# Optimization experiments

Measured on AMD Instinct MI355X. Metric: run time of the kernel, lower is better.

## Reference

```python
import jax, jax.numpy as jnp
import numpy as np

D = 1024
H = 8          # MHA fallback num_heads
DH = D // H
DFF = 4096     # mlp_ratio * hidden_size
EPS = 1e-6


def _ln(x, g, b):
    mu = jnp.mean(x, axis=-1, keepdims=True)
    var = jnp.mean((x - mu) ** 2, axis=-1, keepdims=True)
    return (x - mu) * jax.lax.rsqrt(var + EPS) * g + b


def setup_inputs() -> dict:
    key = jax.random.key(0)
    ks = jax.random.split(key, 16)
    s = 0.02
    return {
        "x": jax.random.normal(ks[0], (8, 1024, D), jnp.float32),
        "c": jax.random.normal(ks[1], (8, D), jnp.float32),
        # Mamba-block (attention fallback) params
        "m_ada_w": jax.random.normal(ks[2], (D, 3 * D), jnp.float32) * s,
        "m_ada_b": jnp.zeros((3 * D,), jnp.float32),
        "m_norm_g": jnp.ones((D,), jnp.float32),
        "m_norm_b": jnp.zeros((D,), jnp.float32),
        "in_proj_w": jax.random.normal(ks[3], (3 * D, D), jnp.float32) * s,
        "in_proj_b": jnp.zeros((3 * D,), jnp.float32),
        "out_proj_w": jax.random.normal(ks[4], (D, D), jnp.float32) * s,
        "out_proj_b": jnp.zeros((D,), jnp.float32),
        # FeedForward-block params
        "f_ada_w": jax.random.normal(ks[5], (D, 3 * D), jnp.float32) * s,
        "f_ada_b": jnp.zeros((3 * D,), jnp.float32),
        "f_norm_g": jnp.ones((D,), jnp.float32),
        "f_norm_b": jnp.zeros((D,), jnp.float32),
        "w1": jax.random.normal(ks[6], (D, DFF), jnp.float32) * s,
        "b1": jnp.zeros((DFF,), jnp.float32),
        "w2": jax.random.normal(ks[7], (DFF, D), jnp.float32) * s,
        "b2": jnp.zeros((D,), jnp.float32),
    }


def reference(x, c, m_ada_w, m_ada_b, m_norm_g, m_norm_b, in_proj_w, in_proj_b,
              out_proj_w, out_proj_b, f_ada_w, f_ada_b, f_norm_g, f_norm_b,
              w1, b1, w2, b2):
    B, N, _ = x.shape
    # ---- MambaBlock (MHA fallback), dropout = identity (eval) ----
    mod = jax.nn.silu(c) @ m_ada_w + m_ada_b              # (B, 3D)
    shift, scale, gate = jnp.split(mod, 3, axis=-1)
    h = _ln(x, m_norm_g, m_norm_b)
    h = h * (1.0 + scale[:, None, :]) + shift[:, None, :]
    qkv = h @ in_proj_w.T + in_proj_b                      # (B, N, 3D)
    q, k, v = jnp.split(qkv, 3, axis=-1)
    q = q.reshape(B, N, H, DH)
    k = k.reshape(B, N, H, DH)
    v = v.reshape(B, N, H, DH)
    scores = jnp.einsum("bqhd,bkhd->bhqk", q, k) / np.sqrt(DH).astype(np.float32)
    attn = jax.nn.softmax(scores, axis=-1)
    o = jnp.einsum("bhqk,bkhd->bqhd", attn, v).reshape(B, N, D)
    o = o @ out_proj_w.T + out_proj_b
    x = x + gate[:, None, :] * o
    # ---- FeedForward block ----
    mod2 = jax.nn.silu(c) @ f_ada_w + f_ada_b
    shift2, scale2, gate2 = jnp.split(mod2, 3, axis=-1)
    h = _ln(x, f_norm_g, f_norm_b)
    h = h * (1.0 + scale2[:, None, :]) + shift2[:, None, :]
    h = jax.nn.gelu(h @ w1 + b1, approximate=False) @ w2 + b2
    return x + gate2[:, None, :] * h
```

## Files before the change

### kernel.cpp

```cpp
#include <hip/hip_runtime.h>

typedef __bf16 bf16x8 __attribute__((ext_vector_type(8)));
typedef float f32x4 __attribute__((ext_vector_type(4)));

__device__ __forceinline__ unsigned short f2bf(float f) {
    unsigned int u = __float_as_uint(f);
    unsigned int r = (u + 0x7FFFu + ((u >> 16) & 1u)) >> 16;
    return (unsigned short)r;
}

__device__ __forceinline__ void gload16(const void* g, void* l) {
    __builtin_amdgcn_global_load_lds(
        (const __attribute__((address_space(1))) unsigned int*)g,
        (__attribute__((address_space(3))) unsigned int*)l, 16, 0, 0);
}

__device__ __forceinline__ void barrier_raw() {
    asm volatile("" ::: "memory");
    __builtin_amdgcn_s_barrier();
    asm volatile("" ::: "memory");
}

__device__ __forceinline__ void vmwait0() {
    asm volatile("s_waitcnt vmcnt(0)" ::: "memory");
}

__device__ __forceinline__ float gelu_fast(float u) {
    float z = 1.595769122f * u + 0.071354816f * u * u * u;
    return u / (1.f + __expf(-z));
}

__global__ __launch_bounds__(256) void f2b4(const float* __restrict__ in,
                                            unsigned short* __restrict__ out) {
    size_t i = ((size_t)blockIdx.x * 256 + threadIdx.x) * 4;
    float4 v = *(const float4*)(in + i);
    ushort4 o;
    o.x = f2bf(v.x); o.y = f2bf(v.y); o.z = f2bf(v.z); o.w = f2bf(v.w);
    *(ushort4*)(out + i) = o;
}

__global__ __launch_bounds__(256) void transpose_f2b(const float* __restrict__ in,
                                                     unsigned short* __restrict__ out,
                                                     int R, int C) {
    __shared__ float tile[32][33];
    int r0 = blockIdx.y * 32, c0 = blockIdx.x * 32;
    int tx = threadIdx.x & 31, ty = threadIdx.x >> 5;
#pragma unroll
    for (int i = 0; i < 4; i++) {
        int r = ty + i * 8;
        tile[r][tx] = in[(size_t)(r0 + r) * C + c0 + tx];
    }
    __syncthreads();
#pragma unroll
    for (int i = 0; i < 4; i++) {
        int r = ty + i * 8;
        out[(size_t)(c0 + r) * R + r0 + tx] = f2bf(tile[tx][r]);
    }
}

__global__ __launch_bounds__(256) void ada_mod_part(const float* __restrict__ c,
                                                    const float* __restrict__ W,
                                                    float* __restrict__ partial) {
    __shared__ float sc[8 * 64];
    int kc = blockIdx.y * 64;
    for (int i = threadIdx.x; i < 512; i += 256) {
        int b = i >> 6, k = i & 63;
        float cv = c[b * 1024 + kc + k];
        sc[i] = cv / (1.f + __expf(-cv));
    }
    __syncthreads();
    int j = blockIdx.x * 256 + threadIdx.x;
    float acc[8] = {0, 0, 0, 0, 0, 0, 0, 0};
    for (int k = 0; k < 64; k++) {
        float w = W[(size_t)(kc + k) * 3072 + j];
#pragma unroll
        for (int b = 0; b < 8; b++) acc[b] += sc[b * 64 + k] * w;
    }
#pragma unroll
    for (int b = 0; b < 8; b++) partial[((size_t)blockIdx.y * 8 + b) * 3072 + j] = acc[b];
}

__global__ __launch_bounds__(256) void ada_reduce(const float* __restrict__ partial,
                                                  const float* __restrict__ bias,
                                                  float* __restrict__ out) {
    int idx = blockIdx.x * 256 + threadIdx.x;
    int b = idx / 3072;
    int jj = idx - b * 3072;
    float s = bias[jj];
#pragma unroll
    for (int ch = 0; ch < 16; ch++) s += partial[((size_t)ch * 8 + b) * 3072 + jj];
    out[idx] = s;
}

__global__ __launch_bounds__(256) void ln_mod_kernel(const float* __restrict__ x,
                                                     const float* __restrict__ gamma,
                                                     const float* __restrict__ beta,
                                                     const float* __restrict__ mods,
                                                     unsigned short* __restrict__ out) {
    int row = blockIdx.x;
    int b = row >> 10;
    float4 v = ((const float4*)(x + (size_t)row * 1024))[threadIdx.x];
    float s = v.x + v.y + v.z + v.w;
    float s2 = v.x * v.x + v.y * v.y + v.z * v.z + v.w * v.w;
#pragma unroll
    for (int d = 1; d < 64; d <<= 1) { s += __shfl_xor(s, d); s2 += __shfl_xor(s2, d); }
    __shared__ float red[8];
    int lane = threadIdx.x & 63, wid = threadIdx.x >> 6;
    if (lane == 0) { red[wid] = s; red[4 + wid] = s2; }
    __syncthreads();
    float S = red[0] + red[1] + red[2] + red[3];
    float S2 = red[4] + red[5] + red[6] + red[7];
    float mu = S * (1.f / 1024.f);
    float var = S2 * (1.f / 1024.f) - mu * mu;
    float rs = rsqrtf(var + 1e-6f);
    const float* mrow = mods + b * 3072;
    int j0 = threadIdx.x * 4;
    float hv[4] = {v.x, v.y, v.z, v.w};
    ushort4 o;
    unsigned short* op = (unsigned short*)&o;
#pragma unroll
    for (int i = 0; i < 4; i++) {
        int j = j0 + i;
        float hh = (hv[i] - mu) * rs * gamma[j] + beta[j];
        hh = hh * (1.f + mrow[1024 + j]) + mrow[j];
        op[i] = f2bf(hh);
    }
    *(ushort4*)(out + (size_t)row * 1024 + j0) = o;
}

template <int NF, int EP>
__global__ __launch_bounds__(NF * 128, 4) void gemmo(const unsigned short* __restrict__ A,
                                                     const unsigned short* __restrict__ Bt,
                                                     int N, int K, int nx,
                                                     const float* __restrict__ bias,
                                                     const float* __restrict__ xres,
                                                     const float* __restrict__ mods,
                                                     float* __restrict__ outf,
                                                     unsigned short* __restrict__ outb,
                                                     unsigned short* __restrict__ vt) {
    constexpr int AE = 128 * 32;
    constexpr int BE = NF * 64 * 32;
    extern __shared__ __align__(16) char smem[];
    __bf16* As = (__bf16*)smem;
    __bf16* Bs = As + 2 * AE;

    int tid = threadIdx.x, lane = tid & 63, wid = tid >> 6;
    int wr, wc;
    if (NF == 4) { wr = wid >> 2; wc = wid & 3; }
    else         { wr = wid >> 1; wc = wid & 1; }
    int t = lane & 15, g = lane >> 4;
    int xk2 = ((t >> 1) & 3) * 8;

    int nwg = gridDim.x, chunk = nwg >> 3;
    int swz = (blockIdx.x & 7) * chunk + (blockIdx.x >> 3);
    int bx = swz % nx, by = swz / nx;
    int rowA0 = by * 128, colB0 = bx * (NF * 64);

    int rin = tid >> 2, cblk = tid & 3;
    int scol = (cblk ^ ((rin >> 1) & 3)) * 8;

    auto stage = [&](int nb, int kt) {
        int k0 = kt << 5;
        if (NF == 4) {
            gload16(A + (size_t)(rowA0 + rin) * K + k0 + scol, As + nb * AE + tid * 8);
            gload16(Bt + (size_t)(colB0 + rin) * K + k0 + scol, Bs + nb * BE + tid * 8);
            gload16(Bt + (size_t)(colB0 + 128 + rin) * K + k0 + scol,
                    Bs + nb * BE + 4096 + tid * 8);
        } else {
            gload16(A + (size_t)(rowA0 + rin) * K + k0 + scol, As + nb * AE + tid * 8);
            gload16(A + (size_t)(rowA0 + 64 + rin) * K + k0 + scol,
                    As + nb * AE + 2048 + tid * 8);
            gload16(Bt + (size_t)(colB0 + rin) * K + k0 + scol, Bs + nb * BE + tid * 8);
            gload16(Bt + (size_t)(colB0 + 64 + rin) * K + k0 + scol,
                    Bs + nb * BE + 2048 + tid * 8);
        }
    };

    f32x4 acc[4][4];
#pragma unroll
    for (int m = 0; m < 4; m++)
#pragma unroll
        for (int n = 0; n < 4; n++) acc[m][n] = (f32x4){0.f, 0.f, 0.f, 0.f};

    stage(0, 0);
    vmwait0();
    barrier_raw();

    int NT = K >> 5;
#pragma unroll 2
    for (int kt = 0; kt < NT; ++kt) {
        const __bf16* Ac = As + (kt & 1) * AE;
        const __bf16* Bc = Bs + (kt & 1) * BE;
        bool more = (kt + 1) < NT;
        if (more) stage((kt & 1) ^ 1, kt + 1);

        bf16x8 a[4], b[4];
#pragma unroll
        for (int m = 0; m < 4; m++)
            a[m] = *(const bf16x8*)&Ac[(wr * 64 + m * 16 + t) * 32 + ((g * 8) ^ xk2)];
#pragma unroll
        for (int n = 0; n < 4; n++)
            b[n] = *(const bf16x8*)&Bc[(wc * 64 + n * 16 + t) * 32 + ((g * 8) ^ xk2)];

        __builtin_amdgcn_s_setprio(1);
#pragma unroll
        for (int m = 0; m < 4; m++)
#pragma unroll
            for (int n = 0; n < 4; n++)
                acc[m][n] = __builtin_amdgcn_mfma_f32_16x16x32_bf16(a[m], b[n], acc[m][n], 0, 0, 0);
        __builtin_amdgcn_s_setprio(0);

        if (more) {
            vmwait0();
            barrier_raw();
        }
    }

    int row0 = rowA0 + wr * 64, col0 = colB0 + wc * 64;
    bool vpart = (EP == 0) && (colB0 >= 2048);
#pragma unroll
    for (int m = 0; m < 4; m++)
#pragma unroll
        for (int n = 0; n < 4; n++) {
            int col = col0 + n * 16 + t;
            if (EP == 0 && vpart) {
                int hcol = col - 2048;
                int hh = hcol >> 7, d = hcol & 127;
                int bb = row0 >> 10;
                int ntok = (row0 + m * 16 + g * 4) & 1023;
                float bs = bias[col];
                ushort4 vv;
                vv.x = f2bf(acc[m][n][0] + bs);
                vv.y = f2bf(acc[m][n][1] + bs);
                vv.z = f2bf(acc[m][n][2] + bs);
                vv.w = f2bf(acc[m][n][3] + bs);
                *(ushort4*)(vt + (((size_t)(bb * 8 + hh) * 128 + d) * 1024 + ntok)) = vv;
            } else {
#pragma unroll
                for (int r = 0; r < 4; r++) {
                    int row = row0 + m * 16 + g * 4 + r;
                    float v = acc[m][n][r];
                    if (EP == 0) {
                        outb[(size_t)row * N + col] = f2bf(v + bias[col]);
                    } else if (EP == 1) {
                        int bb = row >> 10;
                        float gt = mods[bb * 3072 + 2048 + col];
                        outf[(size_t)row * 1024 + col] =
                            xres[(size_t)row * 1024 + col] + gt * (v + bias[col]);
                    } else if (EP == 2) {
                        outb[(size_t)row * N + col] = f2bf(gelu_fast(v + bias[col]));
                    } else {
                        int bb = row >> 10;
                        float gt = mods[bb * 3072 + 2048 + col];
                        outf[(size_t)row * 1024 + col] += gt * (v + bias[col]);
                    }
                }
            }
        }
}

__global__ __launch_bounds__(512, 4) void attn_kernel(const unsigned short* __restrict__ qkv,
                                                      const unsigned short* __restrict__ vt,
                                                      unsigned short* __restrict__ o) {
    extern __shared__ __align__(16) char asmem[];
    __bf16* Ks = (__bf16*)asmem;
    __bf16* Vts = Ks + 2 * 64 * 128;

    int bid = blockIdx.x;
    int logical = (bid & 7) * 64 + (bid >> 3);
    int q0 = (logical & 7) * 128;
    int bh = logical >> 3;
    int b = bh >> 3, h = bh & 7;
    int tid = threadIdx.x, lane = tid & 63, w = tid >> 6;
    int t = lane & 15, g = lane >> 4;
    int swzt = (t & 7) << 4;

    const unsigned short* qbase = qkv + (size_t)(b * 1024) * 3072 + h * 128;
    int qrow = q0 + w * 16 + t;
    bf16x8 qf[4];
#pragma unroll
    for (int ks = 0; ks < 4; ks++)
        qf[ks] = *(const bf16x8*)(qbase + (size_t)qrow * 3072 + ks * 32 + g * 8);

    f32x4 Oa[8];
#pragma unroll
    for (int n = 0; n < 8; n++) Oa[n] = (f32x4){0.f, 0.f, 0.f, 0.f};
    float m_r = -1e30f, l_r = 0.f;
    const float scale = 0.08838834764831845f;

    int krow = tid >> 4;
    int ksrc = (((tid & 15) * 16) ^ ((krow & 7) << 4)) >> 1;
    int vrow = tid >> 3;
    int vsrc = (((tid & 7) * 16) ^ ((vrow & 7) << 4)) >> 1;
    const unsigned short* vtg = vt + (size_t)bh * 128 * 1024;

    auto stage = [&](int buf, int kv0) {
        const unsigned short* kb = qkv + (size_t)(b * 1024 + kv0) * 3072 + 1024 + h * 128;
#pragma unroll
        for (int cc = 0; cc < 2; cc++) {
            gload16(kb + (size_t)(cc * 32 + krow) * 3072 + ksrc,
                    (void*)(Ks + buf * 8192 + cc * 4096 + tid * 8));
            gload16(vtg + (size_t)(cc * 64 + vrow) * 1024 + kv0 + vsrc,
                    (void*)(Vts + buf * 8192 + cc * 4096 + tid * 8));
        }
    };

    stage(0, 0);
    vmwait0();
    barrier_raw();

#pragma unroll 1
    for (int tile = 0; tile < 16; ++tile) {
        int cur = tile & 1;
        bool more = tile < 15;
        if (more) stage(cur ^ 1, (tile + 1) * 64);
        const __bf16* Kc = Ks + cur * 8192;
        const __bf16* Vc = Vts + cur * 8192;

        f32x4 St[4];
#pragma unroll
        for (int n = 0; n < 4; n++) St[n] = (f32x4){0.f, 0.f, 0.f, 0.f};
        __builtin_amdgcn_s_setprio(1);
#pragma unroll
        for (int ks = 0; ks < 4; ks++) {
#pragma unroll
            for (int n = 0; n < 4; n++) {
                bf16x8 kf = *(const bf16x8*)&Kc[(n * 16 + t) * 128 + (((ks * 64 + g * 16) ^ swzt) >> 1)];
                St[n] = __builtin_amdgcn_mfma_f32_16x16x32_bf16(kf, qf[ks], St[n], 0, 0, 0);
            }
        }
        __builtin_amdgcn_s_setprio(0);

        float mx = -1e30f;
#pragma unroll
        for (int n = 0; n < 4; n++)
#pragma unroll
            for (int r = 0; r < 4; r++) mx = fmaxf(mx, St[n][r]);
        mx *= scale;
        mx = fmaxf(mx, __shfl_xor(mx, 16));
        mx = fmaxf(mx, __shfl_xor(mx, 32));
        float mn = fmaxf(m_r, mx);
        float alpha = __expf(m_r - mn);
        m_r = mn;
        float p[4][4];
        float rs = 0.f;
#pragma unroll
        for (int n = 0; n < 4; n++)
#pragma unroll
            for (int r = 0; r < 4; r++) {
                float pv = __expf(St[n][r] * scale - mn);
                p[n][r] = pv;
                rs += pv;
            }
        rs += __shfl_xor(rs, 16);
        rs += __shfl_xor(rs, 32);
        l_r = l_r * alpha + rs;

        unsigned P01[4], P23[4];
#pragma unroll
        for (int n = 0; n < 4; n++) {
            P01[n] = (unsigned)f2bf(p[n][0]) | ((unsigned)f2bf(p[n][1]) << 16);
            P23[n] = (unsigned)f2bf(p[n][2]) | ((unsigned)f2bf(p[n][3]) << 16);
        }

#pragma unroll
        for (int r = 0; r < 4; r++) {
            float ar = __shfl(alpha, (lane & 48) + g * 4 + r);
#pragma unroll
            for (int n2 = 0; n2 < 8; n2++) Oa[n2][r] *= ar;
        }

#pragma unroll
        for (int ks2 = 0; ks2 < 2; ks2++) {
            int e = ks2 * 2, od = ks2 * 2 + 1;
            unsigned s16a = (g < 2) ? P01[e] : P01[od];
            unsigned s16b = (g < 2) ? P23[e] : P23[od];
            unsigned s32a = (g & 1) ? P01[e] : P01[od];
            unsigned s32b = (g & 1) ? P23[e] : P23[od];
            unsigned s48a = (g >= 2) ? P01[e] : P01[od];
            unsigned s48b = (g >= 2) ? P23[e] : P23[od];
            unsigned r16a = __shfl_xor(s16a, 16), r16b = __shfl_xor(s16b, 16);
            unsigned r32a = __shfl_xor(s32a, 32), r32b = __shfl_xor(s32b, 32);
            unsigned r48a = __shfl_xor(s48a, 48), r48b = __shfl_xor(s48b, 48);
            union { unsigned u[4]; bf16x8 v; } pa;
            pa.u[0] = (g == 0) ? P01[e] : (g == 1) ? r48a : (g == 2) ? r32a : r16a;
            pa.u[1] = (g == 0) ? P23[e] : (g == 1) ? r48b : (g == 2) ? r32b : r16b;
            pa.u[2] = (g == 0) ? r16a : (g == 1) ? r32a : (g == 2) ? r48a : P01[od];
            pa.u[3] = (g == 0) ? r16b : (g == 1) ? r32b : (g == 2) ? r48b : P23[od];
            __builtin_amdgcn_s_setprio(1);
#pragma unroll
            for (int n2 = 0; n2 < 8; n2++) {
                bf16x8 vf = *(const bf16x8*)&Vc[(n2 * 16 + t) * 64 + (((ks2 * 64 + g * 16) ^ swzt) >> 1)];
                Oa[n2] = __builtin_amdgcn_mfma_f32_16x16x32_bf16(pa.v, vf, Oa[n2], 0, 0, 0);
            }
            __builtin_amdgcn_s_setprio(0);
        }

        if (more) {
            vmwait0();
            barrier_raw();
        }
    }

#pragma unroll
    for (int r = 0; r < 4; r++) {
        float lq = __shfl(l_r, (lane & 48) + g * 4 + r);
        float inv = 1.f / lq;
        int orow = q0 + w * 16 + g * 4 + r;
#pragma unroll
        for (int n2 = 0; n2 < 8; n2++)
            o[(size_t)(b * 1024 + orow) * 1024 + h * 128 + n2 * 16 + t] = f2bf(Oa[n2][r] * inv);
    }
}

extern "C" void kernel_launch(void* const* d_in, const int* in_sizes, int n_in,
                              void* d_out, int out_size, void* d_ws, size_t ws_size,
                              hipStream_t stream) {
    const float* x          = (const float*)d_in[0];
    const float* c          = (const float*)d_in[1];
    const float* m_ada_w    = (const float*)d_in[2];
    const float* m_ada_b    = (const float*)d_in[3];
    const float* m_norm_g   = (const float*)d_in[4];
    const float* m_norm_b   = (const float*)d_in[5];
    const float* in_proj_w  = (const float*)d_in[6];
    const float* in_proj_b  = (const float*)d_in[7];
    const float* out_proj_w = (const float*)d_in[8];
    const float* out_proj_b = (const float*)d_in[9];
    const float* f_ada_w    = (const float*)d_in[10];
    const float* f_ada_b    = (const float*)d_in[11];
    const float* f_norm_g   = (const float*)d_in[12];
    const float* f_norm_b   = (const float*)d_in[13];
    const float* w1         = (const float*)d_in[14];
    const float* b1         = (const float*)d_in[15];
    const float* w2         = (const float*)d_in[16];
    const float* b2         = (const float*)d_in[17];
    float* out = (float*)d_out;
    char* ws = (char*)d_ws;

    unsigned short* Wq   = (unsigned short*)(ws + 0);
    unsigned short* Wo   = (unsigned short*)(ws + 6291456);
    unsigned short* vt   = (unsigned short*)(ws + 8388608);
    unsigned short* W1t  = (unsigned short*)(ws + 8388608);
    unsigned short* W2t  = (unsigned short*)(ws + 16777216);
    float*          modm = (float*)(ws + 25165824);
    float*          modf = (float*)(ws + 25264128);
    unsigned short* hbuf = (unsigned short*)(ws + 25362432);
    float*          part = (float*)(ws + 25362432);
    float*          part2= (float*)(ws + 25362432 + 2097152);
    unsigned short* qkv  = (unsigned short*)(ws + 42139648);
    unsigned short* obuf = (unsigned short*)(ws + 92471296);
    unsigned short* h2   = (unsigned short*)(ws + 42139648);

    hipFuncSetAttribute((const void*)&gemmo<4, 0>, hipFuncAttributeMaxDynamicSharedMemorySize, 49152);
    hipFuncSetAttribute((const void*)&gemmo<4, 2>, hipFuncAttributeMaxDynamicSharedMemorySize, 49152);
    hipFuncSetAttribute((const void*)&gemmo<2, 1>, hipFuncAttributeMaxDynamicSharedMemorySize, 32768);
    hipFuncSetAttribute((const void*)&gemmo<2, 3>, hipFuncAttributeMaxDynamicSharedMemorySize, 32768);
    hipFuncSetAttribute((const void*)&attn_kernel, hipFuncAttributeMaxDynamicSharedMemorySize, 65536);

    hipLaunchKernelGGL(ada_mod_part, dim3(12, 16), dim3(256), 0, stream, c, m_ada_w, part);
    hipLaunchKernelGGL(ada_mod_part, dim3(12, 16), dim3(256), 0, stream, c, f_ada_w, part2);
    hipLaunchKernelGGL(ada_reduce, dim3(96), dim3(256), 0, stream, part, m_ada_b, modm);
    hipLaunchKernelGGL(ada_reduce, dim3(96), dim3(256), 0, stream, part2, f_ada_b, modf);

    hipLaunchKernelGGL(f2b4, dim3(3072), dim3(256), 0, stream, in_proj_w, Wq);
    hipLaunchKernelGGL(f2b4, dim3(1024), dim3(256), 0, stream, out_proj_w, Wo);

    hipLaunchKernelGGL(ln_mod_kernel, dim3(8192), dim3(256), 0, stream, x, m_norm_g, m_norm_b, modm, hbuf);
    hipLaunchKernelGGL(HIP_KERNEL_NAME(gemmo<4, 0>), dim3(768), dim3(512), 49152, stream,
                       hbuf, Wq, 3072, 1024, 12, in_proj_b, (const float*)nullptr,
                       (const float*)nullptr, (float*)nullptr, qkv, vt);
    hipLaunchKernelGGL(attn_kernel, dim3(512), dim3(512), 65536, stream, qkv, vt, obuf);
    hipLaunchKernelGGL(HIP_KERNEL_NAME(gemmo<2, 1>), dim3(512), dim3(256), 32768, stream,
                       obuf, Wo, 1024, 1024, 8, out_proj_b, x, modm, out,
                       (unsigned short*)nullptr, (unsigned short*)nullptr);

    hipLaunchKernelGGL(transpose_f2b, dim3(128, 32), dim3(256), 0, stream, w1, W1t, 1024, 4096);
    hipLaunchKernelGGL(transpose_f2b, dim3(32, 128), dim3(256), 0, stream, w2, W2t, 4096, 1024);

    hipLaunchKernelGGL(ln_mod_kernel, dim3(8192), dim3(256), 0, stream, out, f_norm_g, f_norm_b, modf, hbuf);
    hipLaunchKernelGGL(HIP_KERNEL_NAME(gemmo<4, 2>), dim3(1024), dim3(512), 49152, stream,
                       hbuf, W1t, 4096, 1024, 16, b1, (const float*)nullptr,
                       (const float*)nullptr, (float*)nullptr, h2, (unsigned short*)nullptr);
    hipLaunchKernelGGL(HIP_KERNEL_NAME(gemmo<2, 3>), dim3(512), dim3(256), 32768, stream,
                       h2, W2t, 1024, 4096, 8, b2, (const float*)nullptr, modf, out,
                       (unsigned short*)nullptr, (unsigned short*)nullptr);
}
```

Baseline: 385.8 us.

## Use 4-wave 128x256 GEMM tiles with 128x64 per-wave outputs for QKV and FC1

Splits the GEMM into two kernels. The wide GEMMs (QKV projection and FC1) now use 256 threads (4 waves), each wave computing a 128x64 output slab with 8x4 MFMA accumulators, instead of 512 threads with 64x64 per wave. The block-to-tile mapping now walks rows fastest (ny = 64), changing which tiles run together and so L2 reuse. This raises MFMA work per LDS B-fragment load but doubles accumulator registers and cuts occupancy (launch bounds 256,2), risking register pressure or lower latency hiding.

```diff
diff --git a/kernel.cpp b/kernel.cpp
--- a/kernel.cpp
+++ b/kernel.cpp
@@ -128,57 +128,45 @@
     *(ushort4*)(out + (size_t)row * 1024 + j0) = o;
 }
 
-template <int NF, int EP>
-__global__ __launch_bounds__(NF * 128, 4) void gemmo(const unsigned short* __restrict__ A,
-                                                     const unsigned short* __restrict__ Bt,
-                                                     int N, int K, int nx,
-                                                     const float* __restrict__ bias,
-                                                     const float* __restrict__ xres,
-                                                     const float* __restrict__ mods,
-                                                     float* __restrict__ outf,
-                                                     unsigned short* __restrict__ outb,
-                                                     unsigned short* __restrict__ vt) {
+template <int EP>
+__global__ __launch_bounds__(256, 2) void gemmw(const unsigned short* __restrict__ A,
+                                                const unsigned short* __restrict__ Bt,
+                                                int N, int K, int ny,
+                                                const float* __restrict__ bias,
+                                                unsigned short* __restrict__ outb,
+                                                unsigned short* __restrict__ vt) {
     constexpr int AE = 128 * 32;
-    constexpr int BE = NF * 64 * 32;
+    constexpr int BE = 256 * 32;
     extern __shared__ __align__(16) char smem[];
     __bf16* As = (__bf16*)smem;
     __bf16* Bs = As + 2 * AE;
 
     int tid = threadIdx.x, lane = tid & 63, wid = tid >> 6;
-    int wr, wc;
-    if (NF == 4) { wr = wid >> 2; wc = wid & 3; }
-    else         { wr = wid >> 1; wc = wid & 1; }
     int t = lane & 15, g = lane >> 4;
     int xk2 = ((t >> 1) & 3) * 8;
 
     int nwg = gridDim.x, chunk = nwg >> 3;
     int swz = (blockIdx.x & 7) * chunk + (blockIdx.x >> 3);
-    int bx = swz % nx, by = swz / nx;
-    int rowA0 = by * 128, colB0 = bx * (NF * 64);
+    int bx = swz / ny, by = swz % ny;
+    int rowA0 = by * 128, colB0 = bx * 256;
 
     int rin = tid >> 2, cblk = tid & 3;
     int scol = (cblk ^ ((rin >> 1) & 3)) * 8;
 
     auto stage = [&](int nb, int kt) {
         int k0 = kt << 5;
-        if (NF == 4) {
-            gload16(A + (size_t)(rowA0 + rin) * K + k0 + scol, As + nb * AE + tid * 8);
-            gload16(Bt + (size_t)(colB0 + rin) * K + k0 + scol, Bs + nb * BE + tid * 8);
-            gload16(Bt + (size_t)(colB0 + 128 + rin) * K + k0 + scol,
-                    Bs + nb * BE + 4096 + tid * 8);
-        } else {
-            gload16(A + (size_t)(rowA0 + rin) * K + k0 + scol, As + nb * AE + tid * 8);
-            gload16(A + (size_t)(rowA0 + 64 + rin) * K + k0 + scol,
-                    As + nb * AE + 2048 + tid * 8);
-            gload16(Bt + (size_t)(colB0 + rin) * K + k0 + scol, Bs + nb * BE + tid * 8);
-            gload16(Bt + (size_t)(colB0 + 64 + rin) * K + k0 + scol,
-                    Bs + nb * BE + 2048 + tid * 8);
-        }
+        gload16(A + (size_t)(rowA0 + rin) * K + k0 + scol, As + nb * AE + tid * 8);
+        gload16(A + (size_t)(rowA0 + 64 + rin) * K + k0 + scol,
+                As + nb * AE + 2048 + tid * 8);
+#pragma unroll
+        for (int sl = 0; sl < 4; sl++)
+            gload16(Bt + (size_t)(colB0 + sl * 64 + rin) * K + k0 + scol,
+                    Bs + nb * BE + sl * 2048 + tid * 8);
     };
 
-    f32x4 acc[4][4];
-#pragma unroll
-    for (int m = 0; m < 4; m++)
+    f32x4 acc[8][4];
+#pragma unroll
+    for (int m = 0; m < 8; m++)
 #pragma unroll
         for (int n = 0; n < 4; n++) acc[m][n] = (f32x4){0.f, 0.f, 0.f, 0.f};
 
@@ -194,20 +182,25 @@
         bool more = (kt + 1) < NT;
         if (more) stage((kt & 1) ^ 1, kt + 1);
 
-        bf16x8 a[4], b[4];
-#pragma unroll
-        for (int m = 0; m < 4; m++)
-            a[m] = *(const bf16x8*)&Ac[(wr * 64 + m * 16 + t) * 32 + ((g * 8) ^ xk2)];
+        bf16x8 b[4];
 #pragma unroll
         for (int n = 0; n < 4; n++)
-            b[n] = *(const bf16x8*)&Bc[(wc * 64 + n * 16 + t) * 32 + ((g * 8) ^ xk2)];
+            b[n] = *(const bf16x8*)&Bc[(wid * 64 + n * 16 + t) * 32 + ((g * 8) ^ xk2)];
 
         __builtin_amdgcn_s_setprio(1);
 #pragma unroll
-        for (int m = 0; m < 4; m++)
-#pragma unroll
-            for (int n = 0; n < 4; n++)
-                acc[m][n] = __builtin_amdgcn_mfma_f32_16x16x32_bf16(a[m], b[n], acc[m][n], 0, 0, 0);
+        for (int mh = 0; mh < 2; mh++) {
+            bf16x8 a[4];
+#pragma unroll
+            for (int m4 = 0; m4 < 4; m4++)
+                a[m4] = *(const bf16x8*)&Ac[(mh * 64 + m4 * 16 + t) * 32 + ((g * 8) ^ xk2)];
+#pragma unroll
+            for (int m4 = 0; m4 < 4; m4++)
+#pragma unroll
+                for (int n = 0; n < 4; n++)
+                    acc[mh * 4 + m4][n] =
+                        __builtin_amdgcn_mfma_f32_16x16x32_bf16(a[m4], b[n], acc[mh * 4 + m4][n], 0, 0, 0);
+        }
         __builtin_amdgcn_s_setprio(0);
 
         if (more) {
@@ -216,18 +209,18 @@
         }
     }
 
-    int row0 = rowA0 + wr * 64, col0 = colB0 + wc * 64;
+    int col0 = colB0 + wid * 64;
     bool vpart = (EP == 0) && (colB0 >= 2048);
 #pragma unroll
-    for (int m = 0; m < 4; m++)
+    for (int m = 0; m < 8; m++)
 #pragma unroll
         for (int n = 0; n < 4; n++) {
             int col = col0 + n * 16 + t;
             if (EP == 0 && vpart) {
                 int hcol = col - 2048;
                 int hh = hcol >> 7, d = hcol & 127;
-                int bb = row0 >> 10;
-                int ntok = (row0 + m * 16 + g * 4) & 1023;
+                int bb = rowA0 >> 10;
+                int ntok = (rowA0 + m * 16 + g * 4) & 1023;
                 float bs = bias[col];
                 ushort4 vv;
                 vv.x = f2bf(acc[m][n][0] + bs);
@@ -238,22 +231,112 @@
             } else {
 #pragma unroll
                 for (int r = 0; r < 4; r++) {
-                    int row = row0 + m * 16 + g * 4 + r;
+                    int row = rowA0 + m * 16 + g * 4 + r;
                     float v = acc[m][n][r];
                     if (EP == 0) {
                         outb[(size_t)row * N + col] = f2bf(v + bias[col]);
-                    } else if (EP == 1) {
-                        int bb = row >> 10;
-                        float gt = mods[bb * 3072 + 2048 + col];
-                        outf[(size_t)row * 1024 + col] =
-                            xres[(size_t)row * 1024 + col] + gt * (v + bias[col]);
-                    } else if (EP == 2) {
+                    } else {
                         outb[(size_t)row * N + col] = f2bf(gelu_fast(v + bias[col]));
-                    } else {
-                        int bb = row >> 10;
-                        float gt = mods[bb * 3072 + 2048 + col];
-                        outf[(size_t)row * 1024 + col] += gt * (v + bias[col]);
                     }
+                }
+            }
+        }
+}
+
+template <int EP>
+__global__ __launch_bounds__(256, 4) void gemmo(const unsigned short* __restrict__ A,
+                                                const unsigned short* __restrict__ Bt,
+                                                int N, int K, int nx,
+                                                const float* __restrict__ bias,
+                                                const float* __restrict__ xres,
+                                                const float* __restrict__ mods,
+                                                float* __restrict__ outf) {
+    constexpr int AE = 128 * 32;
+    constexpr int BE = 128 * 32;
+    extern __shared__ __align__(16) char smem[];
+    __bf16* As = (__bf16*)smem;
+    __bf16* Bs = As + 2 * AE;
+
+    int tid = threadIdx.x, lane = tid & 63, wid = tid >> 6;
+    int wr = wid >> 1, wc = wid & 1;
+    int t = lane & 15, g = lane >> 4;
+    int xk2 = ((t >> 1) & 3) * 8;
+
+    int nwg = gridDim.x, chunk = nwg >> 3;
+    int swz = (blockIdx.x & 7) * chunk + (blockIdx.x >> 3);
+    int bx = swz % nx, by = swz / nx;
+    int rowA0 = by * 128, colB0 = bx * 128;
+
+    int rin = tid >> 2, cblk = tid & 3;
+    int scol = (cblk ^ ((rin >> 1) & 3)) * 8;
+
+    auto stage = [&](int nb, int kt) {
+        int k0 = kt << 5;
+        gload16(A + (size_t)(rowA0 + rin) * K + k0 + scol, As + nb * AE + tid * 8);
+        gload16(A + (size_t)(rowA0 + 64 + rin) * K + k0 + scol,
+                As + nb * AE + 2048 + tid * 8);
+        gload16(Bt + (size_t)(colB0 + rin) * K + k0 + scol, Bs + nb * BE + tid * 8);
+        gload16(Bt + (size_t)(colB0 + 64 + rin) * K + k0 + scol,
+                Bs + nb * BE + 2048 + tid * 8);
+    };
+
+    f32x4 acc[4][4];
+#pragma unroll
+    for (int m = 0; m < 4; m++)
+#pragma unroll
+        for (int n = 0; n < 4; n++) acc[m][n] = (f32x4){0.f, 0.f, 0.f, 0.f};
+
+    stage(0, 0);
+    vmwait0();
+    barrier_raw();
+
+    int NT = K >> 5;
+#pragma unroll 2
+    for (int kt = 0; kt < NT; ++kt) {
+        const __bf16* Ac = As + (kt & 1) * AE;
+        const __bf16* Bc = Bs + (kt & 1) * BE;
+        bool more = (kt + 1) < NT;
+        if (more) stage((kt & 1) ^ 1, kt + 1);
+
+        bf16x8 a[4], b[4];
+#pragma unroll
+        for (int m = 0; m < 4; m++)
+            a[m] = *(const bf16x8*)&Ac[(wr * 64 + m * 16 + t) * 32 + ((g * 8) ^ xk2)];
+#pragma unroll
+        for (int n = 0; n < 4; n++)
+            b[n] = *(const bf16x8*)&Bc[(wc * 64 + n * 16 + t) * 32 + ((g * 8) ^ xk2)];
+
+        __builtin_amdgcn_s_setprio(1);
+#pragma unroll
+        for (int m = 0; m < 4; m++)
+#pragma unroll
+            for (int n = 0; n < 4; n++)
+                acc[m][n] = __builtin_amdgcn_mfma_f32_16x16x32_bf16(a[m], b[n], acc[m][n], 0, 0, 0);
+        __builtin_amdgcn_s_setprio(0);
+
+        if (more) {
+            vmwait0();
+            barrier_raw();
+        }
+    }
+
+    int row0 = rowA0 + wr * 64, col0 = colB0 + wc * 64;
+#pragma unroll
+    for (int m = 0; m < 4; m++)
+#pragma unroll
+        for (int n = 0; n < 4; n++) {
+            int col = col0 + n * 16 + t;
+#pragma unroll
+            for (int r = 0; r < 4; r++) {
+                int row = row0 + m * 16 + g * 4 + r;
+                float v = acc[m][n][r];
+                int bb = row >> 10;
+                float gt = mods[bb * 3072 + 2048 + col];
+                if (EP == 1) {
+                    outf[(size_t)row * 1024 + col] =
+                        xres[(size_t)row * 1024 + col] + gt * (v + bias[col]);
+                } else {
+                    outf[(size_t)row * 1024 + col] += gt * (v + bias[col]);
                 }
             }
         }
@@ -451,10 +534,10 @@
     unsigned short* obuf = (unsigned short*)(ws + 92471296);
     unsigned short* h2   = (unsigned short*)(ws + 42139648);
 
-    hipFuncSetAttribute((const void*)&gemmo<4, 0>, hipFuncAttributeMaxDynamicSharedMemorySize, 49152);
-    hipFuncSetAttribute((const void*)&gemmo<4, 2>, hipFuncAttributeMaxDynamicSharedMemorySize, 49152);
-    hipFuncSetAttribute((const void*)&gemmo<2, 1>, hipFuncAttributeMaxDynamicSharedMemorySize, 32768);
-    hipFuncSetAttribute((const void*)&gemmo<2, 3>, hipFuncAttributeMaxDynamicSharedMemorySize, 32768);
+    hipFuncSetAttribute((const void*)&gemmw<0>, hipFuncAttributeMaxDynamicSharedMemorySize, 49152);
+    hipFuncSetAttribute((const void*)&gemmw<2>, hipFuncAttributeMaxDynamicSharedMemorySize, 49152);
+    hipFuncSetAttribute((const void*)&gemmo<1>, hipFuncAttributeMaxDynamicSharedMemorySize, 32768);
+    hipFuncSetAttribute((const void*)&gemmo<3>, hipFuncAttributeMaxDynamicSharedMemorySize, 32768);
     hipFuncSetAttribute((const void*)&attn_kernel, hipFuncAttributeMaxDynamicSharedMemorySize, 65536);
 
     hipLaunchKernelGGL(ada_mod_part, dim3(12, 16), dim3(256), 0, stream, c, m_ada_w, part);
@@ -466,22 +549,18 @@
     hipLaunchKernelGGL(f2b4, dim3(1024), dim3(256), 0, stream, out_proj_w, Wo);
 
     hipLaunchKernelGGL(ln_mod_kernel, dim3(8192), dim3(256), 0, stream, x, m_norm_g, m_norm_b, modm, hbuf);
-    hipLaunchKernelGGL(HIP_KERNEL_NAME(gemmo<4, 0>), dim3(768), dim3(512), 49152, stream,
-                       hbuf, Wq, 3072, 1024, 12, in_proj_b, (const float*)nullptr,
-                       (const float*)nullptr, (float*)nullptr, qkv, vt);
+    hipLaunchKernelGGL(HIP_KERNEL_NAME(gemmw<0>), dim3(768), dim3(256), 49152, stream,
+                       hbuf, Wq, 3072, 1024, 64, in_proj_b, qkv, vt);
     hipLaunchKernelGGL(attn_kernel, dim3(512), dim3(512), 65536, stream, qkv, vt, obuf);
-    hipLaunchKernelGGL(HIP_KERNEL_NAME(gemmo<2, 1>), dim3(512), dim3(256), 32768, stream,
-                       obuf, Wo, 1024, 1024, 8, out_proj_b, x, modm, out,
-                       (unsigned short*)nullptr, (unsigned short*)nullptr);
+    hipLaunchKernelGGL(HIP_KERNEL_NAME(gemmo<1>), dim3(512), dim3(256), 32768, stream,
+                       obuf, Wo, 1024, 1024, 8, out_proj_b, x, modm, out);
 
     hipLaunchKernelGGL(transpose_f2b, dim3(128, 32), dim3(256), 0, stream, w1, W1t, 1024, 4096);
     hipLaunchKernelGGL(transpose_f2b, dim3(32, 128), dim3(256), 0, stream, w2, W2t, 4096, 1024);
 
     hipLaunchKernelGGL(ln_mod_kernel, dim3(8192), dim3(256), 0, stream, out, f_norm_g, f_norm_b, modf, hbuf);
-    hipLaunchKernelGGL(HIP_KERNEL_NAME(gemmo<4, 2>), dim3(1024), dim3(512), 49152, stream,
-                       hbuf, W1t, 4096, 1024, 16, b1, (const float*)nullptr,
-                       (const float*)nullptr, (float*)nullptr, h2, (unsigned short*)nullptr);
-    hipLaunchKernelGGL(HIP_KERNEL_NAME(gemmo<2, 3>), dim3(512), dim3(256), 32768, stream,
-                       h2, W2t, 1024, 4096, 8, b2, (const float*)nullptr, modf, out,
-                       (unsigned short*)nullptr, (unsigned short*)nullptr);
-}
+    hipLaunchKernelGGL(HIP_KERNEL_NAME(gemmw<2>), dim3(1024), dim3(256), 49152, stream,
+                       hbuf, W1t, 4096, 1024, 64, b1, h2, (unsigned short*)nullptr);
+    hipLaunchKernelGGL(HIP_KERNEL_NAME(gemmo<3>), dim3(512), dim3(256), 32768, stream,
+                       h2, W2t, 1024, 4096, 8, b2, (const float*)nullptr, modf, out);
+}
```

New measurement: 394.2 us. +2.2%, slower.
